# Kernel optimization log

Measured on AMD Instinct MI355X. Metric: run time of the kernel, lower is better.

The kernel has to match this reference:

```python
import jax, jax.numpy as jnp
import numpy as np

N = 200000
B = 1024          # batch_size (number of graphs/segments)
D = 256           # in_channels
STEPS = 3         # processing_steps


def setup_inputs() -> dict:
    key = jax.random.key(0)
    ks = jax.random.split(key, 6)
    x = jax.random.normal(ks[0], (N, D), dtype=jnp.float32)
    bank_kg = jnp.zeros((1,), dtype=jnp.float32)  # unused by forward
    batch = jnp.sort(jax.random.randint(ks[1], (N,), 0, B, dtype=jnp.int32))
    q_star = jax.random.normal(ks[2], (B, 2 * D), dtype=jnp.float32)
    s = 1.0 / np.sqrt(D)  # PyTorch LSTM init scale
    W_ih = jax.random.uniform(ks[3], (4 * D, 2 * D), jnp.float32, -s, s)
    W_hh = jax.random.uniform(ks[4], (4 * D, D), jnp.float32, -s, s)
    b_ih = jnp.zeros((4 * D,), dtype=jnp.float32)
    b_hh = jnp.zeros((4 * D,), dtype=jnp.float32)
    return {"x": x, "bank_kg": bank_kg, "batch": batch, "q_star": q_star,
            "W_ih": W_ih, "W_hh": W_hh, "b_ih": b_ih, "b_hh": b_hh}


def _lstm_cell(inp, h, c, W_ih, W_hh, b_ih, b_hh):
    # PyTorch gate order: i, f, g, o
    gates = inp @ W_ih.T + b_ih + h @ W_hh.T + b_hh  # [B, 4D]
    i, f, g, o = jnp.split(gates, 4, axis=-1)
    i = jax.nn.sigmoid(i)
    f = jax.nn.sigmoid(f)
    g = jnp.tanh(g)
    o = jax.nn.sigmoid(o)
    c = f * c + i * g
    h = o * jnp.tanh(c)
    return h, c


def _segment_softmax(e, batch, num_segments):
    # numerically stable softmax over nodes grouped by segment id
    emax = jax.ops.segment_max(e, batch, num_segments=num_segments)
    emax = jnp.where(jnp.isfinite(emax), emax, 0.0)  # guard empty segments
    ee = jnp.exp(e - emax[batch])
    denom = jax.ops.segment_sum(ee, batch, num_segments=num_segments)
    return ee / (denom[batch] + 1e-16)


def reference(x, bank_kg, batch, q_star, W_ih, W_hh, b_ih, b_hh):
    del bank_kg  # unused in the original forward
    h = jnp.zeros((B, D), dtype=x.dtype)
    c = jnp.zeros((B, D), dtype=x.dtype)
    for _ in range(STEPS):
        h, c = _lstm_cell(q_star, h, c, W_ih, W_hh, b_ih, b_hh)
        q = h                                       # [B, D]
        e = jnp.sum(x * q[batch], axis=-1)          # [N] attention logits
        a = _segment_softmax(e, batch, B)           # [N]
        r = jax.ops.segment_sum(a[:, None] * x, batch, num_segments=B)  # [B, D]
        q_star = jnp.concatenate([q, r], axis=-1)   # [B, 2D]
    return q_star
```

## Files before the change

kernel.cpp:

```cpp
#include <hip/hip_runtime.h>
#include <hip/hip_bf16.h>
#include <cstdint>


#define NN     200000
#define BSEG   1024
#define DD     256
#define KA     512
#define FOURD  1024

using bf16x8 = __attribute__((ext_vector_type(8))) __bf16;
using f32x4  = __attribute__((ext_vector_type(4))) float;

__device__ __forceinline__ float bf2f(unsigned int u) {
  union { unsigned int i; float f; } v; v.i = (u & 0xffffu) << 16; return v.f;
}
__device__ __forceinline__ unsigned short f2bf(float f) {
  union { float f; unsigned int i; } v; v.f = f;
  unsigned int x = v.i;
  if ((x & 0x7fffffffu) > 0x7f800000u) return (unsigned short)((x >> 16) | 0x40);
  return (unsigned short)((x + 0x7fffu + ((x >> 16) & 1u)) >> 16);
}
__device__ __forceinline__ void split_bf(float f, unsigned short& hi, unsigned short& lo) {
  hi = f2bf(f);
  lo = f2bf(f - bf2f(hi));
}

__global__ void prep_all(const int* __restrict__ batch, int* __restrict__ segs,
                         const float* __restrict__ Wih, const float* __restrict__ Whh,
                         const float* __restrict__ bih, const float* __restrict__ bhh,
                         unsigned short* __restrict__ W1hi, unsigned short* __restrict__ W1lo,
                         unsigned short* __restrict__ W2hi, unsigned short* __restrict__ W2lo,
                         float* __restrict__ bias,
                         const float* __restrict__ qst,
                         unsigned short* __restrict__ Ahi, unsigned short* __restrict__ Alo,
                         float* __restrict__ c) {
  int idx = blockIdx.x * 256 + threadIdx.x;
  if (idx <= BSEG) {
    int lo = 0, hi = NN;
    while (lo < hi) { int mid = (lo + hi) >> 1; if (batch[mid] < idx) lo = mid + 1; else hi = mid; }
    segs[idx] = lo;
  }
  if (idx < FOURD) bias[idx] = bih[idx] + bhh[idx];
  if (idx < FOURD * KA) {
    int j = idx / KA, k = idx - j * KA;
    float w1 = Wih[j * 512 + k];
    float w2 = (k < 256) ? (Wih[j * 512 + k] + Whh[j * 256 + k])
                         : Wih[j * 512 + k];
    unsigned short hi, lo;
    split_bf(w1, hi, lo); W1hi[idx] = hi; W1lo[idx] = lo;
    split_bf(w2, hi, lo); W2hi[idx] = hi; W2lo[idx] = lo;
  }
  if (idx < BSEG * KA) {
    unsigned short hi, lo; split_bf(qst[idx], hi, lo);
    Ahi[idx] = hi; Alo[idx] = lo;
  }
  if (idx < BSEG * DD) c[idx] = 0.f;
}

__global__ __launch_bounds__(256) void gemm_gates(const unsigned short* __restrict__ Ahi,
                                                  const unsigned short* __restrict__ Alo,
                                                  const unsigned short* __restrict__ Whi,
                                                  const unsigned short* __restrict__ Wlo,
                                                  float* __restrict__ gates) {
  int bx = blockIdx.x;
  int m0 = (bx >> 5) << 7;
  int n0 = (bx & 31) << 5;
  int t = threadIdx.x, w = t >> 6, lane = t & 63;
  int r16 = lane & 15, quad = lane >> 4;

  __shared__ unsigned short sWhi[32 * 64];
  __shared__ unsigned short sWlo[32 * 64];

  f32x4 acc[2][2] = {};

  const unsigned short* a0h = Ahi + (size_t)(m0 + 32 * w + r16) * KA + quad * 8;
  const unsigned short* a0l = Alo + (size_t)(m0 + 32 * w + r16) * KA + quad * 8;

  int srow = t >> 3;
  int scb  = t & 7;
  const unsigned short* gwh = Whi + (size_t)(n0 + srow) * KA + scb * 8;
  const unsigned short* gwl = Wlo + (size_t)(n0 + srow) * KA + scb * 8;
  int sdst = srow * 64 + ((scb ^ (srow & 7)) * 8);

  for (int kc = 0; kc < KA; kc += 64) {
    __syncthreads();
    *(bf16x8*)&sWhi[sdst] = *(const bf16x8*)(gwh + kc);
    *(bf16x8*)&sWlo[sdst] = *(const bf16x8*)(gwl + kc);
    __syncthreads();
    #pragma unroll
    for (int ks = 0; ks < 2; ++ks) {
      bf16x8 bh[2], bl[2];
      #pragma unroll
      for (int ni = 0; ni < 2; ++ni) {
        int wr = 16 * ni + r16;
        int off = wr * 64 + (((ks * 4 + quad) ^ (wr & 7)) * 8);
        bh[ni] = *(const bf16x8*)&sWhi[off];
        bl[ni] = *(const bf16x8*)&sWlo[off];
      }
      #pragma unroll
      for (int ms = 0; ms < 2; ++ms) {
        bf16x8 a  = *(const bf16x8*)(a0h + (size_t)ms * 16 * KA + kc + ks * 32);
        bf16x8 al = *(const bf16x8*)(a0l + (size_t)ms * 16 * KA + kc + ks * 32);
        #pragma unroll
        for (int ni = 0; ni < 2; ++ni) {
          acc[ms][ni] = __builtin_amdgcn_mfma_f32_16x16x32_bf16(a,  bh[ni], acc[ms][ni], 0, 0, 0);
          acc[ms][ni] = __builtin_amdgcn_mfma_f32_16x16x32_bf16(a,  bl[ni], acc[ms][ni], 0, 0, 0);
          acc[ms][ni] = __builtin_amdgcn_mfma_f32_16x16x32_bf16(al, bh[ni], acc[ms][ni], 0, 0, 0);
        }
      }
    }
  }
  #pragma unroll
  for (int ms = 0; ms < 2; ++ms)
    #pragma unroll
    for (int ni = 0; ni < 2; ++ni)
      #pragma unroll
      for (int r = 0; r < 4; ++r)
        gates[(size_t)(m0 + 32 * w + 16 * ms + quad * 4 + r) * FOURD
              + n0 + 16 * ni + r16] = acc[ms][ni][r];
}


#define LDG(buf, base) do {                                                 \
    int r0_ = (base);                                                       \
    int r1_ = (base) + 1 < tend ? (base) + 1 : tend - 1;                    \
    int r2_ = (base) + 2 < tend ? (base) + 2 : tend - 1;                    \
    int r3_ = (base) + 3 < tend ? (base) + 3 : tend - 1;                    \
    buf[0] = *(const float4*)(x + (size_t)r0_ * DD + lane * 4);             \
    buf[1] = *(const float4*)(x + (size_t)r1_ * DD + lane * 4);             \
    buf[2] = *(const float4*)(x + (size_t)r2_ * DD + lane * 4);             \
    buf[3] = *(const float4*)(x + (size_t)r3_ * DD + lane * 4);             \
  } while (0)

#define PROC(buf, base) do {                                                \
    float dx_ = buf[0].x*q.x + buf[0].y*q.y + buf[0].z*q.z + buf[0].w*q.w;  \
    float dy_ = buf[1].x*q.x + buf[1].y*q.y + buf[1].z*q.z + buf[1].w*q.w;  \
    float dz_ = buf[2].x*q.x + buf[2].y*q.y + buf[2].z*q.z + buf[2].w*q.w;  \
    float dw_ = buf[3].x*q.x + buf[3].y*q.y + buf[3].z*q.z + buf[3].w*q.w;  \
    _Pragma("unroll")                                                       \
    for (int off_ = 32; off_; off_ >>= 1) {                                 \
      dx_ += __shfl_xor(dx_, off_);                                         \
      dy_ += __shfl_xor(dy_, off_);                                         \
      dz_ += __shfl_xor(dz_, off_);                                         \
      dw_ += __shfl_xor(dw_, off_);                                         \
    }                                                                       \
    if ((base) + 1 >= tend) dy_ = -3.402823466e38f;                         \
    if ((base) + 2 >= tend) dz_ = -3.402823466e38f;                         \
    if ((base) + 3 >= tend) dw_ = -3.402823466e38f;                         \
    float mn_ = fmaxf(fmaxf(fmaxf(dx_, dy_), fmaxf(dz_, dw_)), m);          \
    float al_ = __expf(m - mn_);                                            \
    float w0_ = __expf(dx_ - mn_), w1_ = __expf(dy_ - mn_);                 \
    float w2_ = __expf(dz_ - mn_), w3_ = __expf(dw_ - mn_);                 \
    l = l * al_ + (w0_ + w1_) + (w2_ + w3_);                                \
    v.x = (v.x*al_ + w0_*buf[0].x) + (w1_*buf[1].x + w2_*buf[2].x) + w3_*buf[3].x; \
    v.y = (v.y*al_ + w0_*buf[0].y) + (w1_*buf[1].y + w2_*buf[2].y) + w3_*buf[3].y; \
    v.z = (v.z*al_ + w0_*buf[0].z) + (w1_*buf[1].z + w2_*buf[2].z) + w3_*buf[3].z; \
    v.w = (v.w*al_ + w0_*buf[0].w) + (w1_*buf[1].w + w2_*buf[2].w) + w3_*buf[3].w; \
    m = mn_;                                                                \
  } while (0)

__global__ __launch_bounds__(256) void attn_fused(const float* __restrict__ x,
                                                  const int* __restrict__ segs,
                                                  const float* __restrict__ gates,
                                                  const float* __restrict__ bias,
                                                  float* __restrict__ c,
                                                  unsigned short* __restrict__ Ahi,
                                                  unsigned short* __restrict__ Alo,
                                                  float* __restrict__ qout) {
  int b = blockIdx.x, t = threadIdx.x;
  int w = t >> 6, lane = t & 63;

  const float* g = gates + (size_t)b * FOURD;
  float gi = g[t]       + bias[t];
  float gf = g[256 + t] + bias[256 + t];
  float gg = g[512 + t] + bias[512 + t];
  float go = g[768 + t] + bias[768 + t];
  float ig = 1.f / (1.f + expf(-gi));
  float fg = 1.f / (1.f + expf(-gf));
  float gt = tanhf(gg);
  float og = 1.f / (1.f + expf(-go));
  int cidx = b * DD + t;
  float cn = fg * c[cidx] + ig * gt;
  c[cidx] = cn;
  float hn = og * tanhf(cn);

  __shared__ __align__(16) float sh[DD];
  sh[t] = hn;
  {
    unsigned short hi, lo; split_bf(hn, hi, lo);
    size_t ro = (size_t)b * KA;
    Ahi[ro + t] = hi;  Alo[ro + t] = lo;
    qout[(size_t)b * 512 + t] = hn;
  }
  __syncthreads();

  int s = segs[b], tend = segs[b + 1];
  float4 q = *(const float4*)(sh + lane * 4);

  float m = -3.402823466e38f;
  float l = 0.f;
  float4 v = {0.f, 0.f, 0.f, 0.f};

  int i0 = s + w * 4;
  float4 b0[4], b1[4], b2[4];
  if (i0      < tend) LDG(b0, i0);
  if (i0 + 16 < tend) LDG(b1, i0 + 16);
  if (i0 + 32 < tend) LDG(b2, i0 + 32);
  for (int i = i0; i < tend; i += 48) {
    PROC(b0, i);
    if (i + 48 < tend) LDG(b0, i + 48);
    if (i + 16 < tend) {
      PROC(b1, i + 16);
      if (i + 64 < tend) LDG(b1, i + 64);
      if (i + 32 < tend) {
        PROC(b2, i + 32);
        if (i + 80 < tend) LDG(b2, i + 80);
      }
    }
  }

  __shared__ float sm[4], sl[4];
  __shared__ __align__(16) float sv[4][DD];
  if (lane == 0) { sm[w] = m; sl[w] = l; }
  *(float4*)(&sv[w][lane * 4]) = v;
  __syncthreads();

  float M = fmaxf(fmaxf(sm[0], sm[1]), fmaxf(sm[2], sm[3]));
  if (M < -1e37f) M = 0.f;
  float a0 = __expf(sm[0] - M), a1 = __expf(sm[1] - M);
  float a2 = __expf(sm[2] - M), a3 = __expf(sm[3] - M);
  float L = sl[0] * a0 + sl[1] * a1 + sl[2] * a2 + sl[3] * a3;
  float r = (sv[0][t] * a0 + sv[1][t] * a1 + sv[2][t] * a2 + sv[3][t] * a3)
            / (L + 1e-16f);

  unsigned short hi, lo; split_bf(r, hi, lo);
  size_t ro = (size_t)b * KA;
  Ahi[ro + DD + t] = hi;  Alo[ro + DD + t] = lo;
  qout[(size_t)b * 512 + DD + t] = r;
}

extern "C" void kernel_launch(void* const* d_in, const int* in_sizes, int n_in,
                              void* d_out, int out_size, void* d_ws, size_t ws_size,
                              hipStream_t stream) {
  const float* x    = (const float*)d_in[0];
  const int*   batc = (const int*)d_in[2];
  const float* qst  = (const float*)d_in[3];
  const float* Wih  = (const float*)d_in[4];
  const float* Whh  = (const float*)d_in[5];
  const float* bih  = (const float*)d_in[6];
  const float* bhh  = (const float*)d_in[7];
  float* out = (float*)d_out;

  char* ws = (char*)d_ws;
  size_t off = 0;
  auto alloc = [&](size_t bytes) -> void* {
    void* p = ws + off; off = (off + bytes + 255) & ~(size_t)255; return p;
  };
  int*            segs = (int*)alloc((size_t)(BSEG + 1) * 4);
  unsigned short* W1hi = (unsigned short*)alloc((size_t)FOURD * KA * 2);
  unsigned short* W1lo = (unsigned short*)alloc((size_t)FOURD * KA * 2);
  unsigned short* W2hi = (unsigned short*)alloc((size_t)FOURD * KA * 2);
  unsigned short* W2lo = (unsigned short*)alloc((size_t)FOURD * KA * 2);
  unsigned short* Ahi  = (unsigned short*)alloc((size_t)BSEG * KA * 2);
  unsigned short* Alo  = (unsigned short*)alloc((size_t)BSEG * KA * 2);
  float*          gate = (float*)alloc((size_t)BSEG * FOURD * 4);
  float*          c    = (float*)alloc((size_t)BSEG * DD * 4);
  float*          bias = (float*)alloc((size_t)FOURD * 4);

  prep_all<<<(FOURD * KA + 255) / 256, 256, 0, stream>>>(
      batc, segs, Wih, Whh, bih, bhh, W1hi, W1lo, W2hi, W2lo, bias, qst, Ahi, Alo, c);

  for (int step = 0; step < 3; ++step) {
    const unsigned short* whi = step ? W2hi : W1hi;
    const unsigned short* wlo = step ? W2lo : W1lo;
    gemm_gates<<<256, 256, 0, stream>>>(Ahi, Alo, whi, wlo, gate);
    attn_fused<<<BSEG, 256, 0, stream>>>(x, segs, gate, bias, c, Ahi, Alo, out);
  }
}
```

Baseline: 423.9 us.

## Fuse prep, gate GEMM and attention into one persistent kernel with grid barriers

Replaces the seven launches (prep, three GEMMs, three attention kernels) with a single persistent kernel of 512 blocks. Steps are separated by a hand-written atomic grid barrier, and the LSTM cell state is kept in registers instead of global memory. The GEMM drops LDS staging and reads operands straight from global memory. This removes launch gaps and the round trip for c, but it relies on all 512 blocks being co-resident. It also halves attention parallelism to two segments per block and may lose GEMM efficiency without shared-memory reuse.

Measured after the change: 851.7 us. 101% more time.

```diff
diff --git a/kernel.cpp b/kernel.cpp
--- a/kernel.cpp
+++ b/kernel.cpp
@@ -8,6 +8,7 @@
 #define DD     256
 #define KA     512
 #define FOURD  1024
+#define NBLK   512
 
 using bf16x8 = __attribute__((ext_vector_type(8))) __bf16;
 using f32x4  = __attribute__((ext_vector_type(4))) float;
@@ -26,101 +27,25 @@
   lo = f2bf(f - bf2f(hi));
 }
 
-__global__ void prep_all(const int* __restrict__ batch, int* __restrict__ segs,
-                         const float* __restrict__ Wih, const float* __restrict__ Whh,
-                         const float* __restrict__ bih, const float* __restrict__ bhh,
-                         unsigned short* __restrict__ W1hi, unsigned short* __restrict__ W1lo,
-                         unsigned short* __restrict__ W2hi, unsigned short* __restrict__ W2lo,
-                         float* __restrict__ bias,
-                         const float* __restrict__ qst,
-                         unsigned short* __restrict__ Ahi, unsigned short* __restrict__ Alo,
-                         float* __restrict__ c) {
-  int idx = blockIdx.x * 256 + threadIdx.x;
-  if (idx <= BSEG) {
-    int lo = 0, hi = NN;
-    while (lo < hi) { int mid = (lo + hi) >> 1; if (batch[mid] < idx) lo = mid + 1; else hi = mid; }
-    segs[idx] = lo;
-  }
-  if (idx < FOURD) bias[idx] = bih[idx] + bhh[idx];
-  if (idx < FOURD * KA) {
-    int j = idx / KA, k = idx - j * KA;
-    float w1 = Wih[j * 512 + k];
-    float w2 = (k < 256) ? (Wih[j * 512 + k] + Whh[j * 256 + k])
-                         : Wih[j * 512 + k];
-    unsigned short hi, lo;
-    split_bf(w1, hi, lo); W1hi[idx] = hi; W1lo[idx] = lo;
-    split_bf(w2, hi, lo); W2hi[idx] = hi; W2lo[idx] = lo;
-  }
-  if (idx < BSEG * KA) {
-    unsigned short hi, lo; split_bf(qst[idx], hi, lo);
-    Ahi[idx] = hi; Alo[idx] = lo;
-  }
-  if (idx < BSEG * DD) c[idx] = 0.f;
-}
-
-__global__ __launch_bounds__(256) void gemm_gates(const unsigned short* __restrict__ Ahi,
-                                                  const unsigned short* __restrict__ Alo,
-                                                  const unsigned short* __restrict__ Whi,
-                                                  const unsigned short* __restrict__ Wlo,
-                                                  float* __restrict__ gates) {
-  int bx = blockIdx.x;
-  int m0 = (bx >> 5) << 7;
-  int n0 = (bx & 31) << 5;
-  int t = threadIdx.x, w = t >> 6, lane = t & 63;
-  int r16 = lane & 15, quad = lane >> 4;
-
-  __shared__ unsigned short sWhi[32 * 64];
-  __shared__ unsigned short sWlo[32 * 64];
-
-  f32x4 acc[2][2] = {};
-
-  const unsigned short* a0h = Ahi + (size_t)(m0 + 32 * w + r16) * KA + quad * 8;
-  const unsigned short* a0l = Alo + (size_t)(m0 + 32 * w + r16) * KA + quad * 8;
-
-  int srow = t >> 3;
-  int scb  = t & 7;
-  const unsigned short* gwh = Whi + (size_t)(n0 + srow) * KA + scb * 8;
-  const unsigned short* gwl = Wlo + (size_t)(n0 + srow) * KA + scb * 8;
-  int sdst = srow * 64 + ((scb ^ (srow & 7)) * 8);
-
-  for (int kc = 0; kc < KA; kc += 64) {
-    __syncthreads();
-    *(bf16x8*)&sWhi[sdst] = *(const bf16x8*)(gwh + kc);
-    *(bf16x8*)&sWlo[sdst] = *(const bf16x8*)(gwl + kc);
-    __syncthreads();
-    #pragma unroll
-    for (int ks = 0; ks < 2; ++ks) {
-      bf16x8 bh[2], bl[2];
-      #pragma unroll
-      for (int ni = 0; ni < 2; ++ni) {
-        int wr = 16 * ni + r16;
-        int off = wr * 64 + (((ks * 4 + quad) ^ (wr & 7)) * 8);
-        bh[ni] = *(const bf16x8*)&sWhi[off];
-        bl[ni] = *(const bf16x8*)&sWlo[off];
-      }
-      #pragma unroll
-      for (int ms = 0; ms < 2; ++ms) {
-        bf16x8 a  = *(const bf16x8*)(a0h + (size_t)ms * 16 * KA + kc + ks * 32);
-        bf16x8 al = *(const bf16x8*)(a0l + (size_t)ms * 16 * KA + kc + ks * 32);
-        #pragma unroll
-        for (int ni = 0; ni < 2; ++ni) {
-          acc[ms][ni] = __builtin_amdgcn_mfma_f32_16x16x32_bf16(a,  bh[ni], acc[ms][ni], 0, 0, 0);
-          acc[ms][ni] = __builtin_amdgcn_mfma_f32_16x16x32_bf16(a,  bl[ni], acc[ms][ni], 0, 0, 0);
-          acc[ms][ni] = __builtin_amdgcn_mfma_f32_16x16x32_bf16(al, bh[ni], acc[ms][ni], 0, 0, 0);
-        }
-      }
+__device__ __forceinline__ void grid_barrier(int* bar, int& gen) {
+  __syncthreads();
+  if (threadIdx.x == 0) {
+    __threadfence();
+    gen++;
+    int prev = __hip_atomic_fetch_add(&bar[0], 1, __ATOMIC_ACQ_REL,
+                                      __HIP_MEMORY_SCOPE_AGENT);
+    if (prev == NBLK - 1) {
+      __hip_atomic_store(&bar[0], 0, __ATOMIC_RELAXED, __HIP_MEMORY_SCOPE_AGENT);
+      __hip_atomic_fetch_add(&bar[1], 1, __ATOMIC_RELEASE,
+                             __HIP_MEMORY_SCOPE_AGENT);
+    } else {
+      while (__hip_atomic_load(&bar[1], __ATOMIC_ACQUIRE,
+                               __HIP_MEMORY_SCOPE_AGENT) < gen)
+        __builtin_amdgcn_s_sleep(2);
     }
   }
-  #pragma unroll
-  for (int ms = 0; ms < 2; ++ms)
-    #pragma unroll
-    for (int ni = 0; ni < 2; ++ni)
-      #pragma unroll
-      for (int r = 0; r < 4; ++r)
-        gates[(size_t)(m0 + 32 * w + 16 * ms + quad * 4 + r) * FOURD
-              + n0 + 16 * ni + r16] = acc[ms][ni][r];
-}
-
+  __syncthreads();
+}
 
 #define LDG(buf, base) do {                                                 \
     int r0_ = (base);                                                       \
@@ -160,84 +85,166 @@
     m = mn_;                                                                \
   } while (0)
 
-__global__ __launch_bounds__(256) void attn_fused(const float* __restrict__ x,
-                                                  const int* __restrict__ segs,
-                                                  const float* __restrict__ gates,
-                                                  const float* __restrict__ bias,
-                                                  float* __restrict__ c,
-                                                  unsigned short* __restrict__ Ahi,
-                                                  unsigned short* __restrict__ Alo,
-                                                  float* __restrict__ qout) {
-  int b = blockIdx.x, t = threadIdx.x;
+__global__ __launch_bounds__(256, 2) void set2set_all(
+    const float* __restrict__ x, const int* __restrict__ batch,
+    const float* __restrict__ qst, const float* __restrict__ Wih,
+    const float* __restrict__ Whh, const float* __restrict__ bih,
+    const float* __restrict__ bhh,
+    int* __restrict__ segs,
+    unsigned short* __restrict__ W1hi, unsigned short* __restrict__ W1lo,
+    unsigned short* __restrict__ W2hi, unsigned short* __restrict__ W2lo,
+    unsigned short* __restrict__ Ahi, unsigned short* __restrict__ Alo,
+    float* __restrict__ gates, int* __restrict__ bar,
+    float* __restrict__ qout) {
+  int k = blockIdx.x, t = threadIdx.x;
   int w = t >> 6, lane = t & 63;
-
-  const float* g = gates + (size_t)b * FOURD;
-  float gi = g[t]       + bias[t];
-  float gf = g[256 + t] + bias[256 + t];
-  float gg = g[512 + t] + bias[512 + t];
-  float go = g[768 + t] + bias[768 + t];
-  float ig = 1.f / (1.f + expf(-gi));
-  float fg = 1.f / (1.f + expf(-gf));
-  float gt = tanhf(gg);
-  float og = 1.f / (1.f + expf(-go));
-  int cidx = b * DD + t;
-  float cn = fg * c[cidx] + ig * gt;
-  c[cidx] = cn;
-  float hn = og * tanhf(cn);
+  int r16 = lane & 15, quad = lane >> 4;
+  int gen = 0;
+
+  int g = k * 256 + t;
+  #pragma unroll
+  for (int rep = 0; rep < 4; ++rep) {
+    int idx = g + rep * (NBLK * 256);
+    int j = idx >> 9, kk = idx & 511;
+    float w1 = Wih[idx];
+    float w2 = (kk < 256) ? w1 + Whh[j * 256 + kk] : w1;
+    unsigned short hi, lo;
+    split_bf(w1, hi, lo); W1hi[idx] = hi; W1lo[idx] = lo;
+    split_bf(w2, hi, lo); W2hi[idx] = hi; W2lo[idx] = lo;
+    float a = qst[idx];
+    split_bf(a, hi, lo); Ahi[idx] = hi; Alo[idx] = lo;
+  }
+  if (g <= BSEG) {
+    int lo = 0, hi = NN;
+    while (lo < hi) { int mid = (lo + hi) >> 1; if (batch[mid] < g) lo = mid + 1; else hi = mid; }
+    segs[g] = lo;
+  }
+  float bi0 = bih[t]       + bhh[t];
+  float bi1 = bih[256 + t] + bhh[256 + t];
+  float bi2 = bih[512 + t] + bhh[512 + t];
+  float bi3 = bih[768 + t] + bhh[768 + t];
+
+  grid_barrier(bar, gen);
+
+  int s0 = segs[2 * k], e0 = segs[2 * k + 1], e1 = segs[2 * k + 2];
+
+  int m0 = (k >> 4) << 5;
+  int n0 = (k & 15) << 6;
+  int arow = m0 + ((w >> 1) << 4) + r16;
+  int bcol = n0 + ((w & 1) << 4) + r16;
 
   __shared__ __align__(16) float sh[DD];
-  sh[t] = hn;
-  {
-    unsigned short hi, lo; split_bf(hn, hi, lo);
-    size_t ro = (size_t)b * KA;
-    Ahi[ro + t] = hi;  Alo[ro + t] = lo;
-    qout[(size_t)b * 512 + t] = hn;
-  }
-  __syncthreads();
-
-  int s = segs[b], tend = segs[b + 1];
-  float4 q = *(const float4*)(sh + lane * 4);
-
-  float m = -3.402823466e38f;
-  float l = 0.f;
-  float4 v = {0.f, 0.f, 0.f, 0.f};
-
-  int i0 = s + w * 4;
-  float4 b0[4], b1[4], b2[4];
-  if (i0      < tend) LDG(b0, i0);
-  if (i0 + 16 < tend) LDG(b1, i0 + 16);
-  if (i0 + 32 < tend) LDG(b2, i0 + 32);
-  for (int i = i0; i < tend; i += 48) {
-    PROC(b0, i);
-    if (i + 48 < tend) LDG(b0, i + 48);
-    if (i + 16 < tend) {
-      PROC(b1, i + 16);
-      if (i + 64 < tend) LDG(b1, i + 64);
-      if (i + 32 < tend) {
-        PROC(b2, i + 32);
-        if (i + 80 < tend) LDG(b2, i + 80);
-      }
-    }
-  }
-
   __shared__ float sm[4], sl[4];
   __shared__ __align__(16) float sv[4][DD];
-  if (lane == 0) { sm[w] = m; sl[w] = l; }
-  *(float4*)(&sv[w][lane * 4]) = v;
-  __syncthreads();
-
-  float M = fmaxf(fmaxf(sm[0], sm[1]), fmaxf(sm[2], sm[3]));
-  if (M < -1e37f) M = 0.f;
-  float a0 = __expf(sm[0] - M), a1 = __expf(sm[1] - M);
-  float a2 = __expf(sm[2] - M), a3 = __expf(sm[3] - M);
-  float L = sl[0] * a0 + sl[1] * a1 + sl[2] * a2 + sl[3] * a3;
-  float r = (sv[0][t] * a0 + sv[1][t] * a1 + sv[2][t] * a2 + sv[3][t] * a3)
-            / (L + 1e-16f);
-
-  unsigned short hi, lo; split_bf(r, hi, lo);
-  size_t ro = (size_t)b * KA;
-  Ahi[ro + DD + t] = hi;  Alo[ro + DD + t] = lo;
-  qout[(size_t)b * 512 + DD + t] = r;
+
+  float c0 = 0.f, c1 = 0.f;
+
+  for (int step = 0; step < 3; ++step) {
+    const unsigned short* Whi_ = step ? W2hi : W1hi;
+    const unsigned short* Wlo_ = step ? W2lo : W1lo;
+
+    {
+      const unsigned short* ah  = Ahi  + (size_t)arow * KA + quad * 8;
+      const unsigned short* al  = Alo  + (size_t)arow * KA + quad * 8;
+      const unsigned short* b0h = Whi_ + (size_t)bcol * KA + quad * 8;
+      const unsigned short* b0l = Wlo_ + (size_t)bcol * KA + quad * 8;
+      const unsigned short* b1h = b0h + (size_t)32 * KA;
+      const unsigned short* b1l = b0l + (size_t)32 * KA;
+      f32x4 acc0 = {}, acc1 = {};
+      #pragma unroll 4
+      for (int kk = 0; kk < 16; ++kk) {
+        bf16x8 a  = *(const bf16x8*)(ah  + kk * 32);
+        bf16x8 aL = *(const bf16x8*)(al  + kk * 32);
+        bf16x8 bh = *(const bf16x8*)(b0h + kk * 32);
+        bf16x8 bl = *(const bf16x8*)(b0l + kk * 32);
+        bf16x8 ch = *(const bf16x8*)(b1h + kk * 32);
+        bf16x8 cl = *(const bf16x8*)(b1l + kk * 32);
+        acc0 = __builtin_amdgcn_mfma_f32_16x16x32_bf16(a,  bh, acc0, 0, 0, 0);
+        acc0 = __builtin_amdgcn_mfma_f32_16x16x32_bf16(a,  bl, acc0, 0, 0, 0);
+        acc0 = __builtin_amdgcn_mfma_f32_16x16x32_bf16(aL, bh, acc0, 0, 0, 0);
+        acc1 = __builtin_amdgcn_mfma_f32_16x16x32_bf16(a,  ch, acc1, 0, 0, 0);
+        acc1 = __builtin_amdgcn_mfma_f32_16x16x32_bf16(a,  cl, acc1, 0, 0, 0);
+        acc1 = __builtin_amdgcn_mfma_f32_16x16x32_bf16(aL, ch, acc1, 0, 0, 0);
+      }
+      int orow = m0 + ((w >> 1) << 4) + (quad << 2);
+      int ocol = n0 + ((w & 1) << 4) + r16;
+      #pragma unroll
+      for (int r = 0; r < 4; ++r) {
+        gates[(size_t)(orow + r) * FOURD + ocol]      = acc0[r];
+        gates[(size_t)(orow + r) * FOURD + ocol + 32] = acc1[r];
+      }
+    }
+    grid_barrier(bar, gen);
+
+    #pragma unroll
+    for (int j = 0; j < 2; ++j) {
+      int b = 2 * k + j;
+      const float* gg_ = gates + (size_t)b * FOURD;
+      float gi = gg_[t]       + bi0;
+      float gf = gg_[256 + t] + bi1;
+      float gg = gg_[512 + t] + bi2;
+      float go = gg_[768 + t] + bi3;
+      float ig = 1.f / (1.f + expf(-gi));
+      float fg = 1.f / (1.f + expf(-gf));
+      float gt = tanhf(gg);
+      float og = 1.f / (1.f + expf(-go));
+      float cn = fg * (j ? c1 : c0) + ig * gt;
+      if (j) c1 = cn; else c0 = cn;
+      float hn = og * tanhf(cn);
+
+      __syncthreads();
+      sh[t] = hn;
+      {
+        unsigned short hi, lo; split_bf(hn, hi, lo);
+        size_t ro = (size_t)b * KA;
+        Ahi[ro + t] = hi;  Alo[ro + t] = lo;
+        qout[(size_t)b * 512 + t] = hn;
+      }
+      __syncthreads();
+
+      int s = j ? e0 : s0, tend = j ? e1 : e0;
+      float4 q = *(const float4*)(sh + lane * 4);
+      float m = -3.402823466e38f;
+      float l = 0.f;
+      float4 v = {0.f, 0.f, 0.f, 0.f};
+
+      int i0 = s + w * 4;
+      float4 b0[4], b1[4], b2[4];
+      if (i0      < tend) LDG(b0, i0);
+      if (i0 + 16 < tend) LDG(b1, i0 + 16);
+      if (i0 + 32 < tend) LDG(b2, i0 + 32);
+      for (int i = i0; i < tend; i += 48) {
+        PROC(b0, i);
+        if (i + 48 < tend) LDG(b0, i + 48);
+        if (i + 16 < tend) {
+          PROC(b1, i + 16);
+          if (i + 64 < tend) LDG(b1, i + 64);
+          if (i + 32 < tend) {
+            PROC(b2, i + 32);
+            if (i + 80 < tend) LDG(b2, i + 80);
+          }
+        }
+      }
+
+      if (lane == 0) { sm[w] = m; sl[w] = l; }
+      *(float4*)(&sv[w][lane * 4]) = v;
+      __syncthreads();
+
+      float M = fmaxf(fmaxf(sm[0], sm[1]), fmaxf(sm[2], sm[3]));
+      if (M < -1e37f) M = 0.f;
+      float a0 = __expf(sm[0] - M), a1 = __expf(sm[1] - M);
+      float a2 = __expf(sm[2] - M), a3 = __expf(sm[3] - M);
+      float L = sl[0] * a0 + sl[1] * a1 + sl[2] * a2 + sl[3] * a3;
+      float r = (sv[0][t] * a0 + sv[1][t] * a1 + sv[2][t] * a2 + sv[3][t] * a3)
+                / (L + 1e-16f);
+
+      unsigned short hi, lo; split_bf(r, hi, lo);
+      size_t ro = (size_t)b * KA;
+      Ahi[ro + DD + t] = hi;  Alo[ro + DD + t] = lo;
+      qout[(size_t)b * 512 + DD + t] = r;
+    }
+    if (step < 2) grid_barrier(bar, gen);
+  }
 }
 
 extern "C" void kernel_launch(void* const* d_in, const int* in_sizes, int n_in,
@@ -257,6 +264,7 @@
   auto alloc = [&](size_t bytes) -> void* {
     void* p = ws + off; off = (off + bytes + 255) & ~(size_t)255; return p;
   };
+  int*            bar  = (int*)alloc(256);
   int*            segs = (int*)alloc((size_t)(BSEG + 1) * 4);
   unsigned short* W1hi = (unsigned short*)alloc((size_t)FOURD * KA * 2);
   unsigned short* W1lo = (unsigned short*)alloc((size_t)FOURD * KA * 2);
@@ -265,16 +273,9 @@
   unsigned short* Ahi  = (unsigned short*)alloc((size_t)BSEG * KA * 2);
   unsigned short* Alo  = (unsigned short*)alloc((size_t)BSEG * KA * 2);
   float*          gate = (float*)alloc((size_t)BSEG * FOURD * 4);
-  float*          c    = (float*)alloc((size_t)BSEG * DD * 4);
-  float*          bias = (float*)alloc((size_t)FOURD * 4);
-
-  prep_all<<<(FOURD * KA + 255) / 256, 256, 0, stream>>>(
-      batc, segs, Wih, Whh, bih, bhh, W1hi, W1lo, W2hi, W2lo, bias, qst, Ahi, Alo, c);
-
-  for (int step = 0; step < 3; ++step) {
-    const unsigned short* whi = step ? W2hi : W1hi;
-    const unsigned short* wlo = step ? W2lo : W1lo;
-    gemm_gates<<<256, 256, 0, stream>>>(Ahi, Alo, whi, wlo, gate);
-    attn_fused<<<BSEG, 256, 0, stream>>>(x, segs, gate, bias, c, Ahi, Alo, out);
-  }
-}
+
+  hipMemsetAsync(bar, 0, 2 * sizeof(int), stream);
+  set2set_all<<<NBLK, 256, 0, stream>>>(
+      x, batc, qst, Wih, Whh, bih, bhh,
+      segs, W1hi, W1lo, W2hi, W2lo, Ahi, Alo, gate, bar, out);
+}
```
